# Optimization experiments

Hardware: AMD Instinct MI355X
Metric: run time of the kernel (lower is better)

Reference implementation:

```python
import jax, jax.numpy as jnp
import numpy as np

CLIP_FRAMES = 16
CLIP_STRIDE = 8
D_CODE = 256
K_CODE = 8192
ENC_DIM = 128 * CLIP_FRAMES * 4 * 4  # 32768
EPS = 1e-5


def setup_inputs() -> dict:
    key = jax.random.key(0)
    ks = jax.random.split(key, 16)
    rn = lambda k, s, sc: (jax.random.normal(k, s, jnp.float32) * sc)
    inp = {}
    inp['x'] = jax.random.normal(ks[0], (4, 3, 64, 96, 96), jnp.float32)
    inp['conv1_w'] = rn(ks[1], (32, 3, 3, 3, 3), 0.1)
    inp['conv1_b'] = jnp.zeros((32,), jnp.float32)
    inp['bn1_g'] = jnp.ones((32,), jnp.float32)
    inp['bn1_b'] = jnp.zeros((32,), jnp.float32)
    inp['conv2_w'] = rn(ks[2], (64, 32, 3, 3, 3), 0.05)
    inp['conv2_b'] = jnp.zeros((64,), jnp.float32)
    inp['bn2_g'] = jnp.ones((64,), jnp.float32)
    inp['bn2_b'] = jnp.zeros((64,), jnp.float32)
    inp['conv3_w'] = rn(ks[3], (128, 64, 3, 3, 3), 0.04)
    inp['conv3_b'] = jnp.zeros((128,), jnp.float32)
    inp['bn3_g'] = jnp.ones((128,), jnp.float32)
    inp['bn3_b'] = jnp.zeros((128,), jnp.float32)
    inp['proj_w'] = rn(ks[4], (D_CODE, ENC_DIM), 0.005)
    inp['proj_b'] = jnp.zeros((D_CODE,), jnp.float32)
    inp['codebook'] = jax.random.uniform(ks[5], (K_CODE, D_CODE), jnp.float32, -1.0 / K_CODE, 1.0 / K_CODE)
    inp['gru_w_ih'] = rn(ks[6], (3 * D_CODE, D_CODE), 0.05)
    inp['gru_w_hh'] = rn(ks[7], (3 * D_CODE, D_CODE), 0.05)
    inp['gru_b_ih'] = jnp.zeros((3 * D_CODE,), jnp.float32)
    inp['gru_b_hh'] = jnp.zeros((3 * D_CODE,), jnp.float32)
    return inp


def _conv3d(x, w, b):
    y = jax.lax.conv_general_dilated(x, w, (1, 1, 1), ((1, 1), (1, 1), (1, 1)),
                                     dimension_numbers=('NCDHW', 'OIDHW', 'NCDHW'))
    return y + b[None, :, None, None, None]


def _bn(x, g, b):
    # training-mode BatchNorm3d: batch stats over (N,D,H,W), biased variance
    m = x.mean(axis=(0, 2, 3, 4), keepdims=True)
    v = ((x - m) ** 2).mean(axis=(0, 2, 3, 4), keepdims=True)
    return g[None, :, None, None, None] * (x - m) * jax.lax.rsqrt(v + EPS) + b[None, :, None, None, None]


def _maxpool(x):
    return jax.lax.reduce_window(x, -jnp.inf, jax.lax.max, (1, 1, 1, 2, 2), (1, 1, 1, 2, 2), 'VALID')


def _adaptive_avgpool(x):
    # [N,128,16,24,24] -> [N,128,16,4,4]; 24/4=6 exact window
    s = jax.lax.reduce_window(x, 0.0, jax.lax.add, (1, 1, 1, 6, 6), (1, 1, 1, 6, 6), 'VALID')
    return s / 36.0


def _gru(xs, w_ih, w_hh, b_ih, b_hh):
    # torch GRU, batch_first, h0=0. xs: [B,L,D]
    B, L, D = xs.shape
    gx = jnp.einsum('bld,gd->blg', xs, w_ih) + b_ih  # [B,L,3D]

    def step(h, gx_t):
        gh = h @ w_hh.T + b_hh
        xr, xz, xn = jnp.split(gx_t, 3, axis=-1)
        hr, hz, hn = jnp.split(gh, 3, axis=-1)
        r = jax.nn.sigmoid(xr + hr)
        z = jax.nn.sigmoid(xz + hz)
        n = jnp.tanh(xn + r * hn)
        h2 = (1.0 - z) * n + z * h
        return h2, h2

    h0 = jnp.zeros((B, D), xs.dtype)
    _, ys = jax.lax.scan(step, h0, jnp.swapaxes(gx, 0, 1))
    return jnp.swapaxes(ys, 0, 1)  # [B,L,D]


def _forward(x, conv1_w, conv1_b, bn1_g, bn1_b, conv2_w, conv2_b, bn2_g, bn2_b,
             conv3_w, conv3_b, bn3_g, bn3_b, proj_w, proj_b, codebook,
             gru_w_ih, gru_w_hh, gru_b_ih, gru_b_hh):
    B, C, T, H, W = x.shape
    num_clips = max(1, (T - CLIP_FRAMES) // CLIP_STRIDE + 1)
    clips = jnp.stack([x[:, :, i * CLIP_STRIDE:i * CLIP_STRIDE + CLIP_FRAMES] for i in range(num_clips)])

    def encode(clip):  # clip: [B,3,16,96,96]; BN stats per-clip like the torch loop
        h = jax.nn.relu(_bn(_conv3d(clip, conv1_w, conv1_b), bn1_g, bn1_b))
        h = _maxpool(h)
        h = jax.nn.relu(_bn(_conv3d(h, conv2_w, conv2_b), bn2_g, bn2_b))
        h = _maxpool(h)
        h = jax.nn.relu(_bn(_conv3d(h, conv3_w, conv3_b), bn3_g, bn3_b))
        h = _adaptive_avgpool(h)            # [B,128,16,4,4]
        h = h.reshape(B, -1)                # [B, 32768]
        return h @ proj_w.T + proj_b        # [B, D_CODE]

    features = jnp.swapaxes(jax.vmap(encode)(clips), 0, 1)  # [B,L,D]
    L, D = features.shape[1], features.shape[2]

    # quantize: squared-Euclidean argmin (same argmin as torch.cdist p=2)
    flat = features.reshape(-1, D)
    d2 = (flat * flat).sum(-1, keepdims=True) - 2.0 * flat @ codebook.T + (codebook * codebook).sum(-1)
    token_indices = jnp.argmin(d2, axis=-1)
    quantized = codebook[token_indices].reshape(B, L, D)

    sg = jax.lax.stop_gradient
    commitment_loss = jnp.mean((features - sg(quantized)) ** 2)
    codebook_loss = jnp.mean((quantized - sg(features)) ** 2)
    context_features = _gru(quantized[:, :-1], gru_w_ih, gru_w_hh, gru_b_ih, gru_b_hh)
    context_loss = jnp.mean((context_features - features[:, 1:]) ** 2)
    vq_loss = commitment_loss + 0.25 * codebook_loss + 0.1 * context_loss
    return token_indices.reshape(B, L), quantized, commitment_loss, codebook_loss, context_loss, vq_loss


def reference(x, conv1_w, conv1_b, bn1_g, bn1_b, conv2_w, conv2_b, bn2_g, bn2_b,
              conv3_w, conv3_b, bn3_g, bn3_b, proj_w, proj_b, codebook,
              gru_w_ih, gru_w_hh, gru_b_ih, gru_b_hh):
    return _forward(x, conv1_w, conv1_b, bn1_g, bn1_b, conv2_w, conv2_b, bn2_g, bn2_b,
                    conv3_w, conv3_b, bn3_g, bn3_b, proj_w, proj_b, codebook,
                    gru_w_ih, gru_w_hh, gru_b_ih, gru_b_hh)
```

## Files before the change

### kernel.cpp

```cpp
#include <hip/hip_runtime.h>
#include <math.h>


typedef __attribute__((ext_vector_type(8))) short short8;
typedef __attribute__((ext_vector_type(4))) float f32x4;

__device__ inline unsigned short f2bf(float x) {
    unsigned int u = __float_as_uint(x);
    u += 0x7FFFu + ((u >> 16) & 1u);
    return (unsigned short)(u >> 16);
}
__device__ inline float bf2f(unsigned short h) {
    return __uint_as_float(((unsigned int)h) << 16);
}
__device__ inline f32x4 vmax4(f32x4 a, f32x4 b) {
    return (f32x4){fmaxf(a.x, b.x), fmaxf(a.y, b.y), fmaxf(a.z, b.z), fmaxf(a.w, b.w)};
}
__device__ inline f32x4 vmin4(f32x4 a, f32x4 b) {
    return (f32x4){fminf(a.x, b.x), fminf(a.y, b.y), fminf(a.z, b.z), fminf(a.w, b.w)};
}

#define MF(d, a, b) d = __builtin_amdgcn_mfma_f32_16x16x32_bf16(a, b, d, 0, 0, 0)

#define C1LOADR(J) \
    f32x4 u = *(const f32x4*)(ip + (J) * 36); \
    f32x4 w4 = *(const f32x4*)(ip + (J) * 36 + 4); \
    f32x4 sA = u; \
    f32x4 sB = __builtin_shufflevector(u, w4, 1, 2, 3, 4); \
    f32x4 sC = __builtin_shufflevector(u, w4, 2, 3, 4, 5);
#define C1UPD0(I) a0_##I += wa0 * sA + wa1 * sB + wa2 * sC; a1_##I += wb0 * sA + wb1 * sB + wb2 * sC;
#define C1UPD1(I) a0_##I += wa3 * sA + wa4 * sB + wa5 * sC; a1_##I += wb3 * sA + wb4 * sB + wb5 * sC;
#define C1UPD2(I) a0_##I += wa6 * sA + wa7 * sB + wa8 * sC; a1_##I += wb6 * sA + wb7 * sB + wb8 * sC;

__launch_bounds__(256, 3)
__global__ void conv1k(const float* __restrict__ x, const float* __restrict__ wgt,
                       const float* __restrict__ bias, float* __restrict__ pmax,
                       float* __restrict__ pmin, float* __restrict__ stats, int t0) {
    int bb = blockIdx.x;
    int xt = bb % 3; int yt = (bb / 3) % 4; int t = (bb / 12) % 16; int n = bb / 192;
    int x0 = xt * 32, y0 = yt * 24;
    __shared__ float tile[9 * 936];
    __shared__ float wl[3456];
    __shared__ float sst[64];
    int tid = threadIdx.x;
    for (int i = tid; i < 3456; i += 256) {
        int idx = i % 12; int r = i / 12;
        int co = r & 31; int p = r >> 5;
        wl[i] = idx < 9 ? wgt[co * 81 + p * 9 + idx] : 0.f;
    }
    if (tid < 64) sst[tid] = 0.f;
    for (int i = tid; i < 7956; i += 256) {
        int p = i / 884; int rem = i % 884;
        int r = rem / 34, cl = rem % 34;
        int ci = p / 3, kt = p % 3;
        int lt = t + kt - 1;
        int yy = y0 + r - 1, xx = x0 + cl - 1;
        float v = 0.f;
        if (lt >= 0 && lt <= 15 && yy >= 0 && yy < 96 && xx >= 0 && xx < 96)
            v = x[((size_t)(n * 3 + ci) * 64 + (t0 + lt)) * 9216 + yy * 96 + cl + x0 - 1];
        tile[p * 936 + r * 36 + cl] = v;
    }
    __syncthreads();

    int cg = tid & 15;
    int co0 = cg * 2;
    float bv0 = bias[co0], bv1 = bias[co0 + 1];
    float ls0 = 0.f, lq0 = 0.f, ls1 = 0.f, lq1 = 0.f;
    size_t nt48 = (size_t)(n * 16 + t) * 48;

    #pragma unroll 1
    for (int rr = 0; rr < 3; ++rr) {
        int sp = rr * 16 + (tid >> 4);
        int tx = sp & 7, ty = sp >> 3;
        f32x4 a0_0 = (f32x4)bv0, a0_1 = (f32x4)bv0, a0_2 = (f32x4)bv0, a0_3 = (f32x4)bv0;
        f32x4 a1_0 = (f32x4)bv1, a1_1 = (f32x4)bv1, a1_2 = (f32x4)bv1, a1_3 = (f32x4)bv1;

        #pragma unroll 1
        for (int p = 0; p < 9; ++p) {
            const float* wpk = wl + ((p * 32 + co0) * 12);
            f32x4 wv0 = *(const f32x4*)(wpk);
            f32x4 wv1 = *(const f32x4*)(wpk + 4);
            f32x4 wv2 = *(const f32x4*)(wpk + 8);
            f32x4 wv3 = *(const f32x4*)(wpk + 12);
            f32x4 wv4 = *(const f32x4*)(wpk + 16);
            f32x4 wv5 = *(const f32x4*)(wpk + 20);
            float wa0 = wv0.x, wa1 = wv0.y, wa2 = wv0.z, wa3 = wv0.w;
            float wa4 = wv1.x, wa5 = wv1.y, wa6 = wv1.z, wa7 = wv1.w;
            float wa8 = wv2.x;
            float wb0 = wv3.x, wb1 = wv3.y, wb2 = wv3.z, wb3 = wv3.w;
            float wb4 = wv4.x, wb5 = wv4.y, wb6 = wv4.z, wb7 = wv4.w;
            float wb8 = wv5.x;
            const float* ip = tile + p * 936 + (ty * 4) * 36 + tx * 4;
            { C1LOADR(0) C1UPD0(0) }
            { C1LOADR(1) C1UPD0(1) C1UPD1(0) }
            { C1LOADR(2) C1UPD0(2) C1UPD1(1) C1UPD2(0) }
            { C1LOADR(3) C1UPD0(3) C1UPD1(2) C1UPD2(1) }
            { C1LOADR(4) C1UPD1(3) C1UPD2(2) }
            { C1LOADR(5) C1UPD2(3) }
        }

        f32x4 s4 = a0_0 + a0_1 + a0_2 + a0_3;
        ls0 += s4.x + s4.y + s4.z + s4.w;
        f32x4 q4 = a0_0 * a0_0 + a0_1 * a0_1 + a0_2 * a0_2 + a0_3 * a0_3;
        lq0 += q4.x + q4.y + q4.z + q4.w;
        f32x4 s5 = a1_0 + a1_1 + a1_2 + a1_3;
        ls1 += s5.x + s5.y + s5.z + s5.w;
        f32x4 q5 = a1_0 * a1_0 + a1_1 * a1_1 + a1_2 * a1_2 + a1_3 * a1_3;
        lq1 += q5.x + q5.y + q5.z + q5.w;

        f32x4 mx0a = vmax4(a0_0, a0_1), mx0b = vmax4(a0_2, a0_3);
        f32x4 mn0a = vmin4(a0_0, a0_1), mn0b = vmin4(a0_2, a0_3);
        f32x4 mx1a = vmax4(a1_0, a1_1), mx1b = vmax4(a1_2, a1_3);
        f32x4 mn1a = vmin4(a1_0, a1_1), mn1b = vmin4(a1_2, a1_3);
        size_t row0 = (nt48 + (size_t)(yt * 12 + ty * 2)) * 1536 + (size_t)(xt * 16 + tx * 2) * 32 + co0;
        size_t row1 = row0 + 1536;
        *(float2*)(pmax + row0)      = make_float2(fmaxf(mx0a.x, mx0a.y), fmaxf(mx1a.x, mx1a.y));
        *(float2*)(pmax + row0 + 32) = make_float2(fmaxf(mx0a.z, mx0a.w), fmaxf(mx1a.z, mx1a.w));
        *(float2*)(pmax + row1)      = make_float2(fmaxf(mx0b.x, mx0b.y), fmaxf(mx1b.x, mx1b.y));
        *(float2*)(pmax + row1 + 32) = make_float2(fmaxf(mx0b.z, mx0b.w), fmaxf(mx1b.z, mx1b.w));
        *(float2*)(pmin + row0)      = make_float2(fminf(mn0a.x, mn0a.y), fminf(mn1a.x, mn1a.y));
        *(float2*)(pmin + row0 + 32) = make_float2(fminf(mn0a.z, mn0a.w), fminf(mn1a.z, mn1a.w));
        *(float2*)(pmin + row1)      = make_float2(fminf(mn0b.x, mn0b.y), fminf(mn1b.x, mn1b.y));
        *(float2*)(pmin + row1 + 32) = make_float2(fminf(mn0b.z, mn0b.w), fminf(mn1b.z, mn1b.w));
    }

    ls0 += __shfl_xor(ls0, 16, 64); ls0 += __shfl_xor(ls0, 32, 64);
    lq0 += __shfl_xor(lq0, 16, 64); lq0 += __shfl_xor(lq0, 32, 64);
    ls1 += __shfl_xor(ls1, 16, 64); ls1 += __shfl_xor(ls1, 32, 64);
    lq1 += __shfl_xor(lq1, 16, 64); lq1 += __shfl_xor(lq1, 32, 64);
    if ((tid & 63) < 16) {
        atomicAdd(&sst[co0 * 2], ls0);
        atomicAdd(&sst[co0 * 2 + 1], lq0);
        atomicAdd(&sst[co0 * 2 + 2], ls1);
        atomicAdd(&sst[co0 * 2 + 3], lq1);
    }
    __syncthreads();
    if (tid < 64) atomicAdd(&stats[tid], sst[tid]);
}

__global__ void bnpool1b(const float* __restrict__ pmax, const float* __restrict__ pmin,
                         const float* __restrict__ st, const float* __restrict__ gam,
                         const float* __restrict__ bet,
                         unsigned short* __restrict__ phi, unsigned short* __restrict__ plo) {
    int i = blockIdx.x * 256 + threadIdx.x;
    int c8 = i & 3; int xo = (i >> 2) % 48; int yo = (i / 192) % 48;
    int t = (i / 9216) % 16; int n = i / 147456;
    size_t base = (((size_t)(n * 16 + t) * 48 + yo) * 48 + xo) * 32 + c8 * 8;
    union { unsigned short s[8]; uint4 v; } Uh, Ul;
    #pragma unroll
    for (int j = 0; j < 8; ++j) {
        int ch = c8 * 8 + j;
        float mean = st[ch * 2] * (1.f / 589824.f);
        float var  = st[ch * 2 + 1] * (1.f / 589824.f) - mean * mean;
        var = var < 0.f ? 0.f : var;
        float sc = gam[ch] / sqrtf(var + 1e-5f);
        float sh = bet[ch] - mean * sc;
        float pv = sc >= 0.f ? pmax[base + j] : pmin[base + j];
        float v = fmaxf(sc * pv + sh, 0.f);
        Uh.s[j] = f2bf(v);
        Ul.s[j] = f2bf(v - bf2f(Uh.s[j]));
    }
    size_t off = ((((size_t)n * 18 + t + 1) * 50 + yo + 1) * 52 + (xo + 1)) * 32 + c8 * 8;
    *(uint4*)(phi + off) = Uh.v;
    *(uint4*)(plo + off) = Ul.v;
}

__launch_bounds__(256, 3)
__global__ void conv2k(const unsigned short* __restrict__ phi, const unsigned short* __restrict__ plo,
                       const unsigned short* __restrict__ w2p, const float* __restrict__ bias,
                       float* __restrict__ out, float* __restrict__ st) {
    __shared__ unsigned short tin[12 * 52 * 40];
    float (*sred)[32] = (float (*)[32])(tin);
    float (*qred)[32] = (float (*)[32])(tin + 256);
    int b = blockIdx.x;
    int k8 = b & 7, i96 = b >> 3;
    int n = k8 >> 1, th = k8 & 1;
    int tt = i96 / 12; int y0 = (i96 - tt * 12) * 4;
    int t = th * 8 + tt;
    int w = threadIdx.x >> 6, lane = threadIdx.x & 63;
    int c = lane & 15, q = lane >> 4;
    int lrow = (w & 1) * 2, h2 = w >> 1;

    f32x4 acc[2][2][3];
    #pragma unroll
    for (int i = 0; i < 2; ++i)
        #pragma unroll
        for (int j = 0; j < 2; ++j)
            #pragma unroll
            for (int k = 0; k < 3; ++k) acc[i][j][k] = (f32x4)0.f;

    const int loff = h2 * 1024 + c * 32 + q * 8;
    int tbo[2][3];
    #pragma unroll
    for (int rr = 0; rr < 2; ++rr)
        #pragma unroll
        for (int xt = 0; xt < 3; ++xt)
            tbo[rr][xt] = ((lrow + rr) * 52 + xt * 16 + c) * 40 + q * 8;

    #pragma unroll 1
    for (int kt = 0; kt < 3; ++kt) {
        const unsigned short* srch = phi + (size_t)(n * 18 + t + kt) * (50 * 52 * 32);
        const unsigned short* srcl = plo + (size_t)(n * 18 + t + kt) * (50 * 52 * 32);
        const unsigned short* wkt = w2p + kt * 36864;
        __syncthreads();
        for (int i = threadIdx.x; i < 2496; i += 256) {
            int g = i & 3; int xx = (i >> 2) % 52; int rh = (i >> 2) / 52;
            int row = rh % 6; int h = rh / 6;
            const unsigned short* src = (h ? srcl : srch) + (size_t)(y0 + row) * 1664 + xx * 32 + g * 8;
            *(uint4*)(tin + (rh * 52 + xx) * 40 + (g << 3)) = *(const uint4*)src;
        }
        __syncthreads();
        #pragma unroll
        for (int ky = 0; ky < 3; ++ky) {
            #pragma unroll
            for (int kx = 0; kx < 3; ++kx) {
                const unsigned short* wb = wkt + (ky * 3 + kx) * 4096 + loff;
                short8 a0 = *(const short8*)(wb);
                short8 a1 = *(const short8*)(wb + 512);
                short8 l0 = *(const short8*)(wb + 2048);
                short8 l1 = *(const short8*)(wb + 2560);
                int off = (ky * 52 + kx) * 40;
                #pragma unroll
                for (int rr = 0; rr < 2; ++rr) {
                    short8 bh0 = *(const short8*)(tin + tbo[rr][0] + off);
                    short8 bl0 = *(const short8*)(tin + tbo[rr][0] + off + 12480);
                    short8 bh1 = *(const short8*)(tin + tbo[rr][1] + off);
                    short8 bl1 = *(const short8*)(tin + tbo[rr][1] + off + 12480);
                    short8 bh2 = *(const short8*)(tin + tbo[rr][2] + off);
                    short8 bl2 = *(const short8*)(tin + tbo[rr][2] + off + 12480);
                    MF(acc[rr][0][0], a0, bh0); MF(acc[rr][0][0], a0, bl0); MF(acc[rr][0][0], l0, bh0);
                    MF(acc[rr][0][1], a0, bh1); MF(acc[rr][0][1], a0, bl1); MF(acc[rr][0][1], l0, bh1);
                    MF(acc[rr][0][2], a0, bh2); MF(acc[rr][0][2], a0, bl2); MF(acc[rr][0][2], l0, bh2);
                    MF(acc[rr][1][0], a1, bh0); MF(acc[rr][1][0], a1, bl0); MF(acc[rr][1][0], l1, bh0);
                    MF(acc[rr][1][1], a1, bh1); MF(acc[rr][1][1], a1, bl1); MF(acc[rr][1][1], l1, bh1);
                    MF(acc[rr][1][2], a1, bh2); MF(acc[rr][1][2], a1, bl2); MF(acc[rr][1][2], l1, bh2);
                }
            }
        }
    }
    __syncthreads();
    #pragma unroll
    for (int mbp = 0; mbp < 2; ++mbp) {
        f32x4 bv = *(const f32x4*)(bias + h2 * 32 + mbp * 16 + q * 4);
        float s0 = 0.f, s1 = 0.f, s2 = 0.f, s3 = 0.f;
        float p0 = 0.f, p1 = 0.f, p2 = 0.f, p3 = 0.f;
        #pragma unroll
        for (int rr = 0; rr < 2; ++rr) {
            int y = y0 + lrow + rr;
            float* ob = out + (((size_t)(n * 16 + t) * 48) + y) * (48 * 64) + h2 * 32 + mbp * 16 + q * 4;
            #pragma unroll
            for (int xt = 0; xt < 3; ++xt) {
                f32x4 v = acc[rr][mbp][xt] + bv;
                *(f32x4*)(ob + (xt * 16 + c) * 64) = v;
                s0 += v.x; s1 += v.y; s2 += v.z; s3 += v.w;
                p0 += v.x * v.x; p1 += v.y * v.y; p2 += v.z * v.z; p3 += v.w * v.w;
            }
        }
        float sv[4] = {s0, s1, s2, s3}, qv[4] = {p0, p1, p2, p3};
        #pragma unroll
        for (int r = 0; r < 4; ++r) {
            float s = sv[r], q2 = qv[r];
            #pragma unroll
            for (int m = 1; m < 16; m <<= 1) { s += __shfl_xor(s, m, 64); q2 += __shfl_xor(q2, m, 64); }
            if (c == 0) { sred[w][mbp * 16 + q * 4 + r] = s; qred[w][mbp * 16 + q * 4 + r] = q2; }
        }
    }
    __syncthreads();
    if (threadIdx.x < 64) {
        int h = threadIdx.x >> 5, loc = threadIdx.x & 31;
        float s = sred[2 * h][loc] + sred[2 * h + 1][loc];
        float q2 = qred[2 * h][loc] + qred[2 * h + 1][loc];
        atomicAdd(&st[threadIdx.x * 2], s);
        atomicAdd(&st[threadIdx.x * 2 + 1], q2);
    }
}

__global__ void bnpool2k(const float* __restrict__ cin, const float* __restrict__ st,
                         const float* __restrict__ gam, const float* __restrict__ bet,
                         unsigned short* __restrict__ phi, unsigned short* __restrict__ plo) {
    int i = blockIdx.x * 256 + threadIdx.x;
    if (i >= 509184) return;
    int oc = i & 7; int xp = (i >> 3) % 34; int yp = (i / 272) % 26;
    int tp = (i / 7072) % 18; int n = i / 127296;
    union { unsigned short s[8]; uint4 v; } Uh, Ul;
    if (tp >= 1 && tp <= 16 && yp >= 1 && yp <= 24 && xp >= 1 && xp <= 24) {
        int t = tp - 1, yo = yp - 1, xo = xp - 1;
        const float* b0 = cin + ((((size_t)(n * 16 + t) * 48) + 2 * yo) * 48 + 2 * xo) * 64 + oc * 8;
        #pragma unroll
        for (int j = 0; j < 8; ++j) {
            int ch = oc * 8 + j;
            float mean = st[ch * 2] * (1.f / 147456.f);
            float var  = st[ch * 2 + 1] * (1.f / 147456.f) - mean * mean;
            var = var < 0.f ? 0.f : var;
            float sc = gam[ch] / sqrtf(var + 1e-5f);
            float sh = bet[ch] - mean * sc;
            float a  = b0[j] * sc + sh;
            float bb = b0[64 + j] * sc + sh;
            float c2 = b0[3072 + j] * sc + sh;
            float d  = b0[3136 + j] * sc + sh;
            float v = fmaxf(fmaxf(fmaxf(a, bb), fmaxf(c2, d)), 0.f);
            Uh.s[j] = f2bf(v);
            Ul.s[j] = f2bf(v - bf2f(Uh.s[j]));
        }
    } else {
        Uh.v = make_uint4(0, 0, 0, 0);
        Ul.v = make_uint4(0, 0, 0, 0);
    }
    size_t off = ((((size_t)n * 18 + tp) * 26 + yp) * 34 + xp) * 64 + oc * 8;
    *(uint4*)(phi + off) = Uh.v;
    *(uint4*)(plo + off) = Ul.v;
}

__launch_bounds__(256, 4)
__global__ void conv3k(const unsigned short* __restrict__ phi, const unsigned short* __restrict__ plo,
                       const unsigned short* __restrict__ w3p, const float* __restrict__ bias,
                       float* __restrict__ out, float* __restrict__ st) {
    __shared__ unsigned short tin[12 * 26 * 64];
    float (*sred)[64] = (float (*)[64])(tin);
    float (*qred)[64] = (float (*)[64])(tin + 512);
    int b = blockIdx.x;
    int k8 = b & 7, i96 = b >> 3;
    int n = k8 >> 1, th = k8 & 1;
    int cg = i96 / 48; int r48 = i96 - cg * 48;
    int tt = r48 / 6;  int y0 = (r48 - tt * 6) * 4;
    int t = th * 8 + tt;
    int wv = threadIdx.x >> 6, lane = threadIdx.x & 63;
    int c = lane & 15, q = lane >> 4;
    int y = y0 + wv;

    f32x4 acc[4][2];
    #pragma unroll
    for (int i = 0; i < 4; ++i) { acc[i][0] = (f32x4)0.f; acc[i][1] = (f32x4)0.f; }

    const unsigned short* wsrc = w3p + (size_t)cg * 221184 + c * 32 + q * 8;

    #pragma unroll 1
    for (int kt = 0; kt < 3; ++kt) {
        const unsigned short* srch = phi + (size_t)(n * 18 + t + kt) * (26 * 34 * 64);
        const unsigned short* srcl = plo + (size_t)(n * 18 + t + kt) * (26 * 34 * 64);
        const unsigned short* wkt = wsrc + kt * 73728;
        __syncthreads();
        for (int i = threadIdx.x; i < 2496; i += 256) {
            int g = i & 7; int xx = (i >> 3) % 26; int rh = (i >> 3) / 26;
            int row = rh % 6; int h = rh / 6;
            const unsigned short* src = (h ? srcl : srch) + (size_t)(y0 + row) * 2176 + xx * 64 + g * 8;
            *(uint4*)(tin + ((rh * 26 + xx) << 6) + ((g ^ (xx & 7)) << 3)) = *(const uint4*)src;
        }
        __syncthreads();
        #pragma unroll 1
        for (int ky = 0; ky < 3; ++ky) {
            int row = wv + ky;
            const unsigned short* wky = wkt + ky * 24576;
            #pragma unroll
            for (int kx = 0; kx < 3; ++kx) {
                #pragma unroll
                for (int kc = 0; kc < 2; ++kc) {
                    const unsigned short* wb = wky + kx * 8192 + kc * 2048;
                    short8 ah[4], al[4], bh[2], bl[2];
                    #pragma unroll
                    for (int mb = 0; mb < 4; ++mb) {
                        ah[mb] = *(const short8*)(wb + mb * 512);
                        al[mb] = *(const short8*)(wb + 4096 + mb * 512);
                    }
                    #pragma unroll
                    for (int xt = 0; xt < 2; ++xt) {
                        int xr = xt * 16 + kx + c;
                        int xx = xr > 25 ? 25 : xr;
                        int so = ((kc * 4 + q) ^ (xx & 7)) << 3;
                        bh[xt] = *(const short8*)(tin + ((row * 26 + xx) << 6) + so);
                        bl[xt] = *(const short8*)(tin + (((6 + row) * 26 + xx) << 6) + so);
                    }
                    #pragma unroll
                    for (int mb = 0; mb < 4; ++mb)
                        #pragma unroll
                        for (int xt = 0; xt < 2; ++xt) {
                            MF(acc[mb][xt], ah[mb], bh[xt]);
                            MF(acc[mb][xt], ah[mb], bl[xt]);
                            MF(acc[mb][xt], al[mb], bh[xt]);
                        }
                }
            }
        }
    }
    __syncthreads();
    float* ob = out + (((size_t)(n * 16 + t) * 24) + y) * (24 * 128) + cg * 64;
    #pragma unroll
    for (int mb = 0; mb < 4; ++mb) {
        f32x4 bv = *(const f32x4*)(bias + cg * 64 + mb * 16 + q * 4);
        f32x4 v0 = acc[mb][0] + bv;
        f32x4 v1 = acc[mb][1] + bv;
        *(f32x4*)(ob + c * 128 + mb * 16 + q * 4) = v0;
        if (c < 8) *(f32x4*)(ob + (16 + c) * 128 + mb * 16 + q * 4) = v1;
        #pragma unroll
        for (int r = 0; r < 4; ++r) {
            float s  = v0[r] + (c < 8 ? v1[r] : 0.f);
            float q2 = v0[r] * v0[r] + (c < 8 ? v1[r] * v1[r] : 0.f);
            #pragma unroll
            for (int m = 1; m < 16; m <<= 1) { s += __shfl_xor(s, m, 64); q2 += __shfl_xor(q2, m, 64); }
            if (c == 0) { sred[wv][mb * 16 + q * 4 + r] = s; qred[wv][mb * 16 + q * 4 + r] = q2; }
        }
    }
    __syncthreads();
    if (threadIdx.x < 64) {
        int co = cg * 64 + threadIdx.x;
        float s = sred[0][threadIdx.x] + sred[1][threadIdx.x] + sred[2][threadIdx.x] + sred[3][threadIdx.x];
        float q2 = qred[0][threadIdx.x] + qred[1][threadIdx.x] + qred[2][threadIdx.x] + qred[3][threadIdx.x];
        atomicAdd(&st[co * 2], s);
        atomicAdd(&st[co * 2 + 1], q2);
    }
}

__global__ void bnavgk(const float* __restrict__ x, const float* __restrict__ st,
                       const float* __restrict__ gam, const float* __restrict__ bet,
                       float* __restrict__ enc) {
    int i = blockIdx.x * 256 + threadIdx.x;
    int c = i & 127; int xo = (i >> 7) & 3; int yo = (i >> 9) & 3;
    int t = (i >> 11) & 15; int n = i >> 15;
    float mean = st[c * 2] * (1.f / 36864.f);
    float var  = st[c * 2 + 1] * (1.f / 36864.f) - mean * mean;
    var = var < 0.f ? 0.f : var;
    float sc = gam[c] / sqrtf(var + 1e-5f);
    float sh = bet[c] - mean * sc;
    const float* base = x + ((((size_t)(n * 16 + t) * 24) + yo * 6) * 24 + xo * 6) * 128 + c;
    float s = 0.f;
    #pragma unroll
    for (int wy = 0; wy < 6; ++wy)
        #pragma unroll
        for (int wx = 0; wx < 6; ++wx)
            s += fmaxf(base[(wy * 24 + wx) * 128] * sc + sh, 0.f);
    enc[(size_t)n * 32768 + (size_t)c * 256 + t * 16 + yo * 4 + xo] = s * (1.f / 36.f);
}

__global__ void prep2k(const float* __restrict__ c2w, unsigned short* __restrict__ w2p) {
    int i = blockIdx.x * 256 + threadIdx.x;
    if (i >= 110592) return;
    int ci = i & 31; int co = (i >> 5) & 63; int h = (i >> 11) & 1;
    int o = (i >> 12) % 9; int kt = i / 36864;
    int ky = o / 3, kx = o % 3;
    float w = c2w[(((size_t)(co * 32 + ci) * 3 + kt) * 3 + ky) * 3 + kx];
    unsigned short hi = f2bf(w);
    w2p[i] = h ? f2bf(w - bf2f(hi)) : hi;
}
__global__ void prep3k(const float* __restrict__ c3w, unsigned short* __restrict__ w3p) {
    int i = blockIdx.x * 256 + threadIdx.x;
    if (i >= 442368) return;
    int cil = i & 31; int cop = (i >> 5) & 63; int kc = (i >> 11) & 1; int h = (i >> 12) & 1;
    int kx = (i >> 13) % 3; int ky = (i / 24576) % 3; int kt = (i / 73728) % 3; int cg = i / 221184;
    int ci = kc * 32 + cil; int co = cg * 64 + cop;
    float w = c3w[(((size_t)(co * 64 + ci) * 3 + kt) * 3 + ky) * 3 + kx];
    unsigned short hi = f2bf(w);
    w3p[i] = h ? f2bf(w - bf2f(hi)) : hi;
}
__global__ void prepwhhk(const float* __restrict__ whh, float* __restrict__ wt) {
    int i = blockIdx.x * 256 + threadIdx.x;
    int g = i % 768, k = i / 768;
    wt[i] = whh[(size_t)g * 256 + k];
}

__global__ void transck(const float* __restrict__ cb, float* __restrict__ cbT) {
    __shared__ float t[32][33];
    int bx = blockIdx.x & 255;
    int by = blockIdx.x >> 8;
    int ld = threadIdx.x & 31, lk = threadIdx.x >> 5;
    #pragma unroll
    for (int i = 0; i < 4; ++i) {
        int kl = lk + i * 8;
        t[kl][ld] = cb[(size_t)(bx * 32 + kl) * 256 + by * 32 + ld];
    }
    __syncthreads();
    #pragma unroll
    for (int i = 0; i < 4; ++i) {
        int dl = lk + i * 8;
        cbT[(size_t)(by * 32 + dl) * 8192 + bx * 32 + ld] = t[ld][dl];
    }
}

__global__ void cnormk(const float* __restrict__ cbT, double* __restrict__ cn2) {
    int k = blockIdx.x * 256 + threadIdx.x;
    double s = 0.0;
    for (int d = 0; d < 256; ++d) {
        double c = (double)cbT[(size_t)d * 8192 + k];
        s += c * c;
    }
    cn2[k] = s;
}

__global__ void projinitk(const float* __restrict__ pb, float* __restrict__ feat) {
    int i = blockIdx.x * 256 + threadIdx.x;
    feat[i] = pb[i & 255];
}

__global__ void projk(const float* __restrict__ enc, const float* __restrict__ pw,
                      float* __restrict__ feat) {
    int d = blockIdx.x & 255; int ch = blockIdx.x >> 8;
    int k0 = ch * 4096;
    float acc[28];
    #pragma unroll
    for (int e = 0; e < 28; ++e) acc[e] = 0.f;
    const float* wrow = pw + (size_t)d * 32768 + k0;
    for (int k = threadIdx.x; k < 4096; k += 256) {
        float wv = wrow[k];
        #pragma unroll
        for (int e = 0; e < 28; ++e) acc[e] += enc[(size_t)e * 32768 + k0 + k] * wv;
    }
    __shared__ float red[4 * 28];
    #pragma unroll
    for (int e = 0; e < 28; ++e) {
        float v = acc[e];
        #pragma unroll
        for (int o = 32; o > 0; o >>= 1) v += __shfl_down(v, o, 64);
        if ((threadIdx.x & 63) == 0) red[(threadIdx.x >> 6) * 28 + e] = v;
    }
    __syncthreads();
    if (threadIdx.x < 28) {
        int e = threadIdx.x;
        int l = e >> 2, n = e & 3;
        float s = red[e] + red[28 + e] + red[56 + e] + red[84 + e];
        atomicAdd(&feat[(size_t)(n * 7 + l) * 256 + d], s);
    }
}

__global__ void quantk(const float* __restrict__ feat, const float* __restrict__ cbT,
                       const double* __restrict__ cn2, unsigned long long* __restrict__ best) {
    int kc = blockIdx.x & 31, r = blockIdx.x >> 5;
    int k = kc * 256 + threadIdx.x;
    __shared__ float fs[256];
    fs[threadIdx.x] = feat[(size_t)r * 256 + threadIdx.x];
    __syncthreads();
    double dot = 0.0;
    for (int d = 0; d < 256; ++d)
        dot += (double)cbT[(size_t)d * 8192 + k] * (double)fs[d];
    float s = (float)(cn2[k] - 2.0 * dot);
    unsigned int bits = __float_as_uint(s);
    unsigned int key = (bits & 0x80000000u) ? ~bits : (bits | 0x80000000u);
    unsigned long long p = ((unsigned long long)key << 32) | (unsigned int)k;
    #pragma unroll
    for (int o = 32; o > 0; o >>= 1) {
        unsigned long long qv = __shfl_down(p, o, 64);
        if (qv < p) p = qv;
    }
    if ((threadIdx.x & 63) == 0) atomicMin(&best[r], p);
}

__global__ void gatherk(const unsigned long long* __restrict__ best,
                        const float* __restrict__ feat, const float* __restrict__ cb,
                        float* __restrict__ dout, float* __restrict__ quant,
                        float* __restrict__ acc) {
    int r = blockIdx.x;
    int d = threadIdx.x;
    int idx = (int)(best[r] & 0xFFFFFFFFull);
    float q = cb[(size_t)idx * 256 + d];
    quant[r * 256 + d] = q;
    dout[28 + r * 256 + d] = q;
    if (d == 0) dout[r] = (float)idx;
    float df = feat[r * 256 + d] - q;
    float v = df * df;
    #pragma unroll
    for (int o = 32; o > 0; o >>= 1) v += __shfl_down(v, o, 64);
    if ((d & 63) == 0) atomicAdd(&acc[0], v);
}

__global__ void gxk(const float* __restrict__ quant, const float* __restrict__ wih,
                    const float* __restrict__ bih, float* __restrict__ gx) {
    int o = blockIdx.x * 256 + threadIdx.x;
    int g = o % 768; int t = (o / 768) % 6; int n = o / (768 * 6);
    const float* q = quant + (size_t)(n * 7 + t) * 256;
    const float* w = wih + (size_t)g * 256;
    float s = bih[g];
    #pragma unroll 4
    for (int d = 0; d < 256; ++d) s += q[d] * w[d];
    gx[o] = s;
}

__global__ void gru_allk(const float* __restrict__ gx, const float* __restrict__ wt,
                         const float* __restrict__ bhh, const float* __restrict__ feat,
                         float* __restrict__ acc) {
    int b = blockIdx.x;
    int d = threadIdx.x;
    __shared__ float hs[256];
    hs[d] = 0.f;
    __syncthreads();
    float ctx = 0.f;
    for (int t = 0; t < 6; ++t) {
        float g0 = bhh[d], g1 = bhh[256 + d], g2 = bhh[512 + d];
        #pragma unroll 4
        for (int k = 0; k < 256; ++k) {
            float hv = hs[k];
            const float* wr = wt + (size_t)k * 768;
            g0 += wr[d] * hv; g1 += wr[256 + d] * hv; g2 += wr[512 + d] * hv;
        }
        const float* gxr = gx + (size_t)(b * 6 + t) * 768;
        float xr = gxr[d], xz = gxr[256 + d], xn = gxr[512 + d];
        float rr = 1.f / (1.f + expf(-(xr + g0)));
        float zz = 1.f / (1.f + expf(-(xz + g1)));
        float nn = tanhf(xn + rr * g2);
        float h2 = (1.f - zz) * nn + zz * hs[d];
        __syncthreads();
        hs[d] = h2;
        __syncthreads();
        float df = h2 - feat[(size_t)(b * 7 + t + 1) * 256 + d];
        ctx += df * df;
    }
    #pragma unroll
    for (int o = 32; o > 0; o >>= 1) ctx += __shfl_down(ctx, o, 64);
    if ((d & 63) == 0) atomicAdd(&acc[1], ctx);
}

__global__ void fink(const float* __restrict__ acc, float* __restrict__ dout) {
    float comm = acc[0] / 7168.f;
    float ctx  = acc[1] / 6144.f;
    dout[7196] = comm;
    dout[7197] = comm;
    dout[7198] = ctx;
    dout[7199] = comm + 0.25f * comm + 0.1f * ctx;
}

extern "C" void kernel_launch(void* const* d_in, const int* in_sizes, int n_in,
                              void* d_out, int out_size, void* d_ws, size_t ws_size,
                              hipStream_t stream) {
    (void)in_sizes; (void)n_in; (void)out_size; (void)ws_size;
    const float* x    = (const float*)d_in[0];
    const float* c1w  = (const float*)d_in[1];
    const float* c1b  = (const float*)d_in[2];
    const float* bn1g = (const float*)d_in[3];
    const float* bn1b = (const float*)d_in[4];
    const float* c2w  = (const float*)d_in[5];
    const float* c2b  = (const float*)d_in[6];
    const float* bn2g = (const float*)d_in[7];
    const float* bn2b = (const float*)d_in[8];
    const float* c3w  = (const float*)d_in[9];
    const float* c3b  = (const float*)d_in[10];
    const float* bn3g = (const float*)d_in[11];
    const float* bn3b = (const float*)d_in[12];
    const float* pw   = (const float*)d_in[13];
    const float* pb   = (const float*)d_in[14];
    const float* cb   = (const float*)d_in[15];
    const float* wih  = (const float*)d_in[16];
    const float* whh  = (const float*)d_in[17];
    const float* bih  = (const float*)d_in[18];
    const float* bhh  = (const float*)d_in[19];
    float* out = (float*)d_out;

    char* w = (char*)d_ws;
    float* A  = (float*)w;                         w += 75497472;
    float* PMAX = A;
    float* PMIN = A + 4718592;
    float* cbT = A;
    double* cn2 = (double*)((char*)A + 8388608);
    char*  SH = w;                                 w += 16293888;
    unsigned short* P3h = (unsigned short*)SH;
    unsigned short* P3l = (unsigned short*)(SH + 8146944);
    unsigned short* P2h = (unsigned short*)w;      w += 11980800;
    unsigned short* P2l = (unsigned short*)w;      w += 11980800;
    unsigned short* W2P = (unsigned short*)w;      w += 221184;
    unsigned short* W3P = (unsigned short*)w;      w += 884736;
    float* WT    = (float*)w;                      w += 786432;
    float* enc   = (float*)w;                      w += 3670016;
    float* feat  = (float*)w;                      w += 28672;
    float* quant = (float*)w;                      w += 28672;
    float* gx    = (float*)w;                      w += 73728;
    float* statsA = (float*)w;                     w += 21504;
    float* acc    = (float*)w;                     w += 16;
    unsigned long long* best = (unsigned long long*)w;  w += 224;

    hipMemsetAsync(P2h, 0, 11980800 * 2, stream);
    hipMemsetAsync(statsA, 0, 21504 + 16, stream);
    hipMemsetAsync(best, 0xFF, 224, stream);
    prep2k<<<432, 256, 0, stream>>>(c2w, W2P);
    prep3k<<<1728, 256, 0, stream>>>(c3w, W3P);
    prepwhhk<<<768, 256, 0, stream>>>(whh, WT);

    for (int l = 0; l < 7; ++l) {
        float* st1 = statsA + (l * 3 + 0) * 256;
        float* st2 = statsA + (l * 3 + 1) * 256;
        float* st3 = statsA + (l * 3 + 2) * 256;
        conv1k<<<768, 256, 0, stream>>>(x, c1w, c1b, PMAX, PMIN, st1, l * 8);
        bnpool1b<<<2304, 256, 0, stream>>>(PMAX, PMIN, st1, bn1g, bn1b, P2h, P2l);
        conv2k<<<768, 256, 0, stream>>>(P2h, P2l, W2P, c2b, A, st2);
        bnpool2k<<<1989, 256, 0, stream>>>(A, st2, bn2g, bn2b, P3h, P3l);
        conv3k<<<768, 256, 0, stream>>>(P3h, P3l, W3P, c3b, A, st3);
        bnavgk<<<512, 256, 0, stream>>>(A, st3, bn3g, bn3b, enc + (size_t)l * 131072);
    }

    transck<<<2048, 256, 0, stream>>>(cb, cbT);
    cnormk<<<32, 256, 0, stream>>>(cbT, cn2);
    projinitk<<<28, 256, 0, stream>>>(pb, feat);
    projk<<<2048, 256, 0, stream>>>(enc, pw, feat);
    quantk<<<896, 256, 0, stream>>>(feat, cbT, cn2, best);
    gatherk<<<28, 256, 0, stream>>>(best, feat, cb, out, quant, acc);
    gxk<<<72, 256, 0, stream>>>(quant, wih, bih, gx);
    gru_allk<<<4, 256, 0, stream>>>(gx, WT, bhh, feat, acc);
    fink<<<1, 1, 0, stream>>>(acc, out);
}
```

Before: 2.209 ms.

## Redistribute conv3 x-remainder columns across waves to avoid wasted MFMA tiles

Each wave used to compute a second 16-column MFMA tile of which only 8 columns were valid. The leftover 8 columns of the four output rows are now packed into full 16-lane tiles shared by wave pairs, with each wave handling half the channel blocks. This removes about a quarter of the MFMA work in the conv3 inner loop. In exchange it adds wave-dependent branching and a more complex output and statistics mapping.

New measurement: 2.208 ms. Within noise of the previous version (-0.0%).

```diff
diff --git a/kernel.cpp b/kernel.cpp
--- a/kernel.cpp
+++ b/kernel.cpp
@@ -327,10 +327,16 @@
     int wv = threadIdx.x >> 6, lane = threadIdx.x & 63;
     int c = lane & 15, q = lane >> 4;
     int y = y0 + wv;
-
-    f32x4 acc[4][2];
-    #pragma unroll
-    for (int i = 0; i < 4; ++i) { acc[i][0] = (f32x4)0.f; acc[i][1] = (f32x4)0.f; }
+    int rp = wv >> 1;
+    int mbr = (wv & 1) * 2;
+    int rbase = rp * 2 + (c >> 3);
+    int xrc = 16 + (c & 7);
+
+    f32x4 accF[4];
+    f32x4 accR[2];
+    #pragma unroll
+    for (int i = 0; i < 4; ++i) accF[i] = (f32x4)0.f;
+    accR[0] = (f32x4)0.f; accR[1] = (f32x4)0.f;
 
     const unsigned short* wsrc = w3p + (size_t)cg * 221184 + c * 32 + q * 8;
 
@@ -349,52 +355,67 @@
         __syncthreads();
         #pragma unroll 1
         for (int ky = 0; ky < 3; ++ky) {
-            int row = wv + ky;
+            int rowF = wv + ky;
+            int rowR = rbase + ky;
             const unsigned short* wky = wkt + ky * 24576;
             #pragma unroll
             for (int kx = 0; kx < 3; ++kx) {
                 #pragma unroll
                 for (int kc = 0; kc < 2; ++kc) {
                     const unsigned short* wb = wky + kx * 8192 + kc * 2048;
-                    short8 ah[4], al[4], bh[2], bl[2];
+                    short8 ah[4], al[4];
                     #pragma unroll
                     for (int mb = 0; mb < 4; ++mb) {
                         ah[mb] = *(const short8*)(wb + mb * 512);
                         al[mb] = *(const short8*)(wb + 4096 + mb * 512);
                     }
+                    int xF = kx + c;
+                    int soF = ((kc * 4 + q) ^ (xF & 7)) << 3;
+                    short8 bhF = *(const short8*)(tin + ((rowF * 26 + xF) << 6) + soF);
+                    short8 blF = *(const short8*)(tin + (((6 + rowF) * 26 + xF) << 6) + soF);
+                    int xR = xrc + kx;
+                    int soR = ((kc * 4 + q) ^ (xR & 7)) << 3;
+                    short8 bhR = *(const short8*)(tin + ((rowR * 26 + xR) << 6) + soR);
+                    short8 blR = *(const short8*)(tin + (((6 + rowR) * 26 + xR) << 6) + soR);
                     #pragma unroll
-                    for (int xt = 0; xt < 2; ++xt) {
-                        int xr = xt * 16 + kx + c;
-                        int xx = xr > 25 ? 25 : xr;
-                        int so = ((kc * 4 + q) ^ (xx & 7)) << 3;
-                        bh[xt] = *(const short8*)(tin + ((row * 26 + xx) << 6) + so);
-                        bl[xt] = *(const short8*)(tin + (((6 + row) * 26 + xx) << 6) + so);
+                    for (int mb = 0; mb < 4; ++mb) {
+                        MF(accF[mb], ah[mb], bhF);
+                        MF(accF[mb], ah[mb], blF);
+                        MF(accF[mb], al[mb], bhF);
                     }
-                    #pragma unroll
-                    for (int mb = 0; mb < 4; ++mb)
-                        #pragma unroll
-                        for (int xt = 0; xt < 2; ++xt) {
-                            MF(acc[mb][xt], ah[mb], bh[xt]);
-                            MF(acc[mb][xt], ah[mb], bl[xt]);
-                            MF(acc[mb][xt], al[mb], bh[xt]);
-                        }
+                    if ((wv & 1) == 0) {
+                        MF(accR[0], ah[0], bhR); MF(accR[0], ah[0], blR); MF(accR[0], al[0], bhR);
+                        MF(accR[1], ah[1], bhR); MF(accR[1], ah[1], blR); MF(accR[1], al[1], bhR);
+                    } else {
+                        MF(accR[0], ah[2], bhR); MF(accR[0], ah[2], blR); MF(accR[0], al[2], bhR);
+                        MF(accR[1], ah[3], bhR); MF(accR[1], ah[3], blR); MF(accR[1], al[3], bhR);
+                    }
                 }
             }
         }
     }
     __syncthreads();
+    f32x4 bvRa = *(const f32x4*)(bias + cg * 64 + mbr * 16 + q * 4);
+    f32x4 bvRb = *(const f32x4*)(bias + cg * 64 + (mbr + 1) * 16 + q * 4);
+    f32x4 vRa = accR[0] + bvRa;
+    f32x4 vRb = accR[1] + bvRb;
+    {
+        float* obr = out + (((size_t)(n * 16 + t) * 24) + y0 + rbase) * (24 * 128)
+                   + cg * 64 + xrc * 128 + q * 4;
+        *(f32x4*)(obr + mbr * 16) = vRa;
+        *(f32x4*)(obr + (mbr + 1) * 16) = vRb;
+    }
     float* ob = out + (((size_t)(n * 16 + t) * 24) + y) * (24 * 128) + cg * 64;
     #pragma unroll
     for (int mb = 0; mb < 4; ++mb) {
         f32x4 bv = *(const f32x4*)(bias + cg * 64 + mb * 16 + q * 4);
-        f32x4 v0 = acc[mb][0] + bv;
-        f32x4 v1 = acc[mb][1] + bv;
+        f32x4 v0 = accF[mb] + bv;
         *(f32x4*)(ob + c * 128 + mb * 16 + q * 4) = v0;
-        if (c < 8) *(f32x4*)(ob + (16 + c) * 128 + mb * 16 + q * 4) = v1;
         #pragma unroll
         for (int r = 0; r < 4; ++r) {
-            float s  = v0[r] + (c < 8 ? v1[r] : 0.f);
-            float q2 = v0[r] * v0[r] + (c < 8 ? v1[r] * v1[r] : 0.f);
+            float ra = (mb == mbr) ? vRa[r] : (mb == mbr + 1) ? vRb[r] : 0.f;
+            float s  = v0[r] + ra;
+            float q2 = v0[r] * v0[r] + ra * ra;
             #pragma unroll
             for (int m = 1; m < 16; m <<= 1) { s += __shfl_xor(s, m, 64); q2 += __shfl_xor(q2, m, 64); }
             if (c == 0) { sred[wv][mb * 16 + q * 4 + r] = s; qred[wv][mb * 16 + q * 4 + r] = q2; }
```
